# Optimization experiments

Hardware: AMD Instinct MI355X
Metric: run time of the kernel (lower is better)

The kernel has to match this reference:

```python
import math
import jax, jax.numpy as jnp
import numpy as np

HIDDEN = 768
HEADS = 12
HEAD_DIM = HIDDEN // HEADS  # 64
NUM_BUCKETS = 32            # T5-style relative position bias defaults
MAX_DIST = 128
EPS = 1e-6


def _rel_buckets(T):
    # T5 bidirectional relative-position bucketing, computed statically in numpy.
    ctx = np.arange(T)[:, None]
    mem = np.arange(T)[None, :]
    rp = mem - ctx                     # (T, T)
    nb = NUM_BUCKETS // 2
    ret = (rp > 0).astype(np.int64) * nb
    n = np.abs(rp)
    max_exact = nb // 2
    is_small = n < max_exact
    val_large = max_exact + (
        np.log(np.maximum(n, 1) / max_exact) / math.log(MAX_DIST / max_exact) * (nb - max_exact)
    ).astype(np.int64)
    val_large = np.minimum(val_large, nb - 1)
    ret = ret + np.where(is_small, n, val_large)
    return ret  # (T, T) int


def _layernorm(x, scale, bias):
    mu = jnp.mean(x, axis=-1, keepdims=True)
    var = jnp.mean((x - mu) ** 2, axis=-1, keepdims=True)
    return (x - mu) * jax.lax.rsqrt(var + EPS) * scale + bias


def _rms_groupnorm(x, weight):
    # x: (N, C, H, W, D); RMS over (channels-in-group, spatial), per-channel scale.
    N, C, H, W, D = x.shape
    xg = x.reshape(N, HEADS, C // HEADS, H, W, D)
    ms = jnp.mean(xg * xg, axis=(2, 3, 4, 5), keepdims=True)
    xg = xg * jax.lax.rsqrt(ms + EPS)
    return xg.reshape(N, C, H, W, D) * weight[None, :, None, None, None]


def _forward(x, norm1_weight, input_head_weight, input_head_bias,
             qnorm_scale, qnorm_bias, knorm_scale, knorm_bias,
             rel_bias_table, output_head_weight, output_head_bias):
    T, B, C, H, W, D = x.shape
    residual = x
    xn = _rms_groupnorm(x.reshape(T * B, C, H, W, D), norm1_weight)
    # 1x1 conv QKV as channels-last matmul
    w_in = input_head_weight[:, :, 0, 0, 0]                       # (3C, C)
    xt = jnp.transpose(xn, (0, 2, 3, 4, 1))                        # (TB, H, W, D, C)
    qkv = xt @ w_in.T + input_head_bias                            # (TB, H, W, D, 3C)
    # '(t b) (he c) h w d -> (b h w d) he t c'  with c = 3*head_dim
    qkv = qkv.reshape(T, B, H, W, D, HEADS, 3 * HEAD_DIM)
    qkv = jnp.transpose(qkv, (1, 2, 3, 4, 5, 0, 6))                # (B,H,W,D,He,T,3hd)
    qkv = qkv.reshape(B * H * W * D, HEADS, T, 3 * HEAD_DIM)
    q, k, v = jnp.split(qkv, 3, axis=-1)                           # each (N, He, T, hd)
    q = _layernorm(q, qnorm_scale, qnorm_bias)
    k = _layernorm(k, knorm_scale, knorm_bias)
    # relative position bias (bidirectional)
    buckets = jnp.asarray(_rel_buckets(T))                         # (T, T)
    bias = jnp.transpose(rel_bias_table[buckets], (2, 0, 1))[None]  # (1, He, T, T)
    scale = 1.0 / math.sqrt(HEAD_DIM)
    attn = jax.nn.softmax(jnp.einsum('bhsc,bhtc->bhst', q, k) * scale + bias, axis=-1)
    out = jnp.einsum('bhst,bhtc->bhsc', attn, v)                   # (N, He, T, hd)
    # '(b h w d) he t c -> (t b) (he c) h w d'
    out = out.reshape(B, H, W, D, HEADS, T, HEAD_DIM)
    out = jnp.transpose(out, (5, 0, 4, 6, 1, 2, 3))                # (T,B,He,hd,H,W,D)
    out = out.reshape(T * B, C, H, W, D)
    # output 1x1 conv
    w_out = output_head_weight[:, :, 0, 0, 0]                      # (C, C)
    ot = jnp.transpose(out, (0, 2, 3, 4, 1)) @ w_out.T + output_head_bias
    y = jnp.transpose(ot, (0, 4, 1, 2, 3)).reshape(T, B, C, H, W, D)
    return y + residual


def setup_inputs() -> dict:
    key = jax.random.key(0)
    ks = jax.random.split(key, 4)
    T, B, C, H, W, D = 16, 1, HIDDEN, 16, 16, 8
    x = jax.random.normal(ks[0], (T, B, C, H, W, D), dtype=jnp.float32)
    lecun = 1.0 / math.sqrt(HIDDEN)
    return {
        'x': x,
        'norm1_weight': jnp.ones((HIDDEN,), jnp.float32),
        'input_head_weight': jax.random.normal(ks[1], (3 * HIDDEN, HIDDEN, 1, 1, 1), jnp.float32) * lecun,
        'input_head_bias': jnp.zeros((3 * HIDDEN,), jnp.float32),
        'qnorm_scale': jnp.ones((HEAD_DIM,), jnp.float32),
        'qnorm_bias': jnp.zeros((HEAD_DIM,), jnp.float32),
        'knorm_scale': jnp.ones((HEAD_DIM,), jnp.float32),
        'knorm_bias': jnp.zeros((HEAD_DIM,), jnp.float32),
        'rel_bias_table': jax.random.normal(ks[2], (NUM_BUCKETS, HEADS), jnp.float32) * 0.02,
        'output_head_weight': jax.random.normal(ks[3], (HIDDEN, HIDDEN, 1, 1, 1), jnp.float32) * lecun,
        'output_head_bias': jnp.zeros((HIDDEN,), jnp.float32),
    }


def reference(x, norm1_weight, input_head_weight, input_head_bias,
              qnorm_scale, qnorm_bias, knorm_scale, knorm_bias,
              rel_bias_table, output_head_weight, output_head_bias):
    return _forward(x, norm1_weight, input_head_weight, input_head_bias,
                    qnorm_scale, qnorm_bias, knorm_scale, knorm_bias,
                    rel_bias_table, output_head_weight, output_head_bias)
```

## Files before the change

kernel.cpp:

```cpp
#include <hip/hip_runtime.h>
#include <stdint.h>

#define Tt 16
#define Cc 768
#define Ss 2048
#define N1 2304
#define NH 12
#define HD 64
#define EPSV 1e-6f

typedef unsigned short ushort_t;
typedef __attribute__((ext_vector_type(8))) short short8;
typedef __attribute__((ext_vector_type(4))) short short4v;
typedef __attribute__((ext_vector_type(4))) float f32x4;

static __device__ __forceinline__ float b2f(unsigned short u) {
  union { unsigned int i; float f; } c;
  c.i = ((unsigned int)u) << 16;
  return c.f;
}
static __device__ __forceinline__ unsigned short f2b(float f) {
  union { float f; unsigned int i; } c;
  c.f = f;
  return (unsigned short)((c.i + 0x7fffu + ((c.i >> 16) & 1u)) >> 16);
}

static __device__ __forceinline__ void load8(const void* p, size_t eoff,
                                             int isf32, float* o) {
  if (isf32) {
    const float* f = (const float*)p + eoff;
    f32x4 a = *(const f32x4*)f;
    f32x4 b = *(const f32x4*)(f + 4);
    o[0] = a[0]; o[1] = a[1]; o[2] = a[2]; o[3] = a[3];
    o[4] = b[0]; o[5] = b[1]; o[6] = b[2]; o[7] = b[3];
  } else {
    short8 d = *(const short8*)((const ushort_t*)p + eoff);
#pragma unroll
    for (int e = 0; e < 8; e++) o[e] = b2f((unsigned short)d[e]);
  }
}
static __device__ __forceinline__ float load1(const void* p, size_t eoff, int isf32) {
  return isf32 ? ((const float*)p)[eoff] : b2f(((const ushort_t*)p)[eoff]);
}

#define GLP(p) ((const __attribute__((address_space(1))) void*)(p))
#define LDSP(p) ((__attribute__((address_space(3))) void*)(p))

__global__ __launch_bounds__(256) void detect_k(const ushort_t* __restrict__ x,
                                               int* __restrict__ flag) {
  __shared__ int sbad;
  if (threadIdx.x == 0) sbad = 0;
  __syncthreads();
  int bad = 0;
  for (int i = threadIdx.x; i < 65536; i += 256) {
    const unsigned int e = (x[i] >> 7) & 0xFFu;
    if (e == 0xFFu) bad = 1;
  }
  if (bad) atomicOr(&sbad, 1);
  __syncthreads();
  if (threadIdx.x == 0) flag[0] = sbad;
}

__global__ __launch_bounds__(256) void cvt_big_k(const void* __restrict__ src,
                                                ushort_t* __restrict__ dst,
                                                int n8, const int* __restrict__ flag) {
  const int isf32 = *flag;
  const int i = blockIdx.x * 256 + threadIdx.x;
  if (i >= n8) return;
  float o[8];
  load8(src, (size_t)i * 8, isf32, o);
  short8 v;
#pragma unroll
  for (int e = 0; e < 8; e++) v[e] = (short)f2b(o[e]);
  *(short8*)(dst + (size_t)i * 8) = v;
}

__global__ __launch_bounds__(256) void cvt_small_k(
    const void* w1, const void* bin, const void* bo, const void* qs,
    const void* qb, const void* ks, const void* kb, const void* relb,
    ushort_t* __restrict__ dst, const int* __restrict__ flag) {
  const int isf32 = *flag;
  const void* srcs[8] = {w1, bin, bo, qs, qb, ks, kb, relb};
  const int sizes[8] = {768, 2304, 768, 64, 64, 64, 64, 384};
  int off = 0;
#pragma unroll
  for (int s = 0; s < 8; s++) {
    for (int i = threadIdx.x; i < sizes[s]; i += 256)
      dst[off + i] = isf32 ? f2b(((const float*)srcs[s])[i])
                           : ((const ushort_t*)srcs[s])[i];
    off += sizes[s];
  }
}

__global__ __launch_bounds__(256) void rms_stats_k(
    const void* __restrict__ x, const int* __restrict__ flag,
    float* __restrict__ invrms) {
  const int isf32 = *flag;
  const int t = blockIdx.x / NH;
  const int g = blockIdx.x % NH;
  const size_t base = ((size_t)(t * Cc + g * 64)) * Ss;
  float ss = 0.f;
  for (int v = threadIdx.x; v < 16384; v += 256) {
    const int ci = v >> 8;
    const int sj = (v & 255) << 3;
    float o[8];
    load8(x, base + (size_t)ci * Ss + sj, isf32, o);
#pragma unroll
    for (int e = 0; e < 8; e++) ss += o[e] * o[e];
  }
#pragma unroll
  for (int m = 1; m < 64; m <<= 1) ss += __shfl_xor(ss, m);
  __shared__ float red[4];
  if ((threadIdx.x & 63) == 0) red[threadIdx.x >> 6] = ss;
  __syncthreads();
  if (threadIdx.x == 0) {
    float tot = red[0] + red[1] + red[2] + red[3];
    invrms[blockIdx.x] = rsqrtf(tot * (1.f / 131072.f) + EPSV);
  }
}

__global__ __launch_bounds__(256) void norm_chunk_k(
    const void* __restrict__ x, const int* __restrict__ flag,
    const ushort_t* __restrict__ w1, const float* __restrict__ invrms,
    ushort_t* __restrict__ xnc, int s0c, int chl) {
  __shared__ __align__(16) ushort_t tile[64][64];
  const int isf32 = *flag;
  const int t = blockIdx.z;
  const int c0 = blockIdx.y * 64;
  const int sl0 = blockIdx.x * 64;
  const float ir = invrms[t * NH + (c0 >> 6)];
  const int tid = threadIdx.x;
  for (int v = tid; v < 512; v += 256) {
    const int ci = v >> 3;
    const int q = v & 7;
    float o[8];
    load8(x, ((size_t)(t * Cc + c0 + ci)) * Ss + s0c + sl0 + q * 8, isf32, o);
    const float sc = ir * b2f(w1[c0 + ci]);
    short8 w;
#pragma unroll
    for (int e = 0; e < 8; e++) w[e] = (short)f2b(o[e] * sc);
    *(short8*)&tile[ci][(q ^ (ci >> 3)) * 8] = w;
  }
  __syncthreads();
  for (int v = tid; v < 512; v += 256) {
    const int sj = v >> 3;
    const int cb = (v & 7) * 8;
    const int sw = (sj >> 3) ^ (v & 7);
    const int so = sj & 7;
    short8 o;
#pragma unroll
    for (int e = 0; e < 8; e++) o[e] = (short)tile[cb + e][sw * 8 + so];
    *(short8*)(xnc + ((size_t)(t * chl + sl0 + sj)) * Cc + c0 + cb) = o;
  }
}

__global__ __launch_bounds__(256, 2) void gemm_qkv_k(
    const ushort_t* __restrict__ A, const ushort_t* __restrict__ Bw,
    const ushort_t* __restrict__ bias, ushort_t* __restrict__ Cout) {
  __shared__ __align__(16) ushort_t As[128 * 32];
  __shared__ __align__(16) ushort_t Bs[128 * 32];
  const int tid = threadIdx.x;
  const int bm0 = blockIdx.x * 128;
  const int bn0 = blockIdx.y * 128;
  const int lane = tid & 63;
  const int wave = tid >> 6;
  const int wm = (wave >> 1) << 6;
  const int wn = (wave & 1) << 6;
  f32x4 acc[4][4];
#pragma unroll
  for (int i = 0; i < 4; i++)
#pragma unroll
    for (int j = 0; j < 4; j++) acc[i][j] = (f32x4){0.f, 0.f, 0.f, 0.f};
  const int srow = tid >> 2;
  const int scol = (tid & 3) << 3;
  const ushort_t* ag = A + (size_t)(bm0 + srow) * Cc + scol;
  const ushort_t* bg = Bw + (size_t)(bn0 + srow) * Cc + scol;
  ushort_t* la = As + tid * 8;
  ushort_t* lb = Bs + tid * 8;
  const int frow = lane & 15;
  const int koff = (lane >> 4) << 3;
  for (int kt = 0; kt < Cc; kt += 32) {
    __syncthreads();
    __builtin_amdgcn_global_load_lds(GLP(ag + kt), LDSP(la), 16, 0, 0);
    __builtin_amdgcn_global_load_lds(GLP(ag + kt + 64 * Cc), LDSP(la + 2048), 16, 0, 0);
    __builtin_amdgcn_global_load_lds(GLP(bg + kt), LDSP(lb), 16, 0, 0);
    __builtin_amdgcn_global_load_lds(GLP(bg + kt + 64 * Cc), LDSP(lb + 2048), 16, 0, 0);
    __syncthreads();
    short8 af[4], bf[4];
#pragma unroll
    for (int i = 0; i < 4; i++)
      af[i] = *(const short8*)(As + (wm + i * 16 + frow) * 32 + koff);
#pragma unroll
    for (int j = 0; j < 4; j++)
      bf[j] = *(const short8*)(Bs + (wn + j * 16 + frow) * 32 + koff);
#pragma unroll
    for (int i = 0; i < 4; i++)
#pragma unroll
      for (int j = 0; j < 4; j++)
        acc[i][j] = __builtin_amdgcn_mfma_f32_16x16x32_bf16(af[i], bf[j], acc[i][j], 0, 0, 0);
  }
  const int mq = (lane >> 4) << 2;
  const int nl = lane & 15;
#pragma unroll
  for (int j = 0; j < 4; j++) {
    const int col = bn0 + wn + j * 16 + nl;
    const float bc = b2f(bias[col]);
#pragma unroll
    for (int i = 0; i < 4; i++) {
#pragma unroll
      for (int r = 0; r < 4; r++) {
        const int row = bm0 + wm + i * 16 + mq + r;
        Cout[(size_t)row * N1 + col] = f2b(acc[i][j][r] + bc);
      }
    }
  }
}

static __device__ __forceinline__ void rdA4(short8 af[4], const ushort_t* base,
                                            int ar, int mib, int ck) {
#pragma unroll
  for (int mi = 0; mi < 4; mi++)
    af[mi] = *(const short8*)&base[(ar + (mib + mi) * 16) * 32 + ck];
}
static __device__ __forceinline__ void rdB4(short8 bf[4], const ushort_t* base,
                                            int br, int ck) {
#pragma unroll
  for (int ni = 0; ni < 4; ni++)
    bf[ni] = *(const short8*)&base[(br + ni * 16) * 32 + ck];
}
template <int MIB>
static __device__ __forceinline__ void mmq(f32x4 (&acc)[8][4], const short8 af[4],
                                           const short8 bf[4]) {
#pragma unroll
  for (int mi = 0; mi < 4; mi++)
#pragma unroll
    for (int ni = 0; ni < 4; ni++)
      acc[MIB + mi][ni] = __builtin_amdgcn_mfma_f32_16x16x32_bf16(
          af[mi], bf[ni], acc[MIB + mi][ni], 0, 0, 0);
}
#define QPH_BAR { __builtin_amdgcn_sched_barrier(0); __builtin_amdgcn_s_barrier(); \
                  __builtin_amdgcn_sched_barrier(0); }
#define LDSOFF(p, ab, kh) ((((p) * 2 + (ab)) * 2 + (kh)) * 8192)

__global__ __launch_bounds__(512, 2) void gemm_qkv256_k(
    const ushort_t* __restrict__ A, const ushort_t* __restrict__ Bw,
    const ushort_t* __restrict__ bias, ushort_t* __restrict__ Cout) {
  __shared__ __align__(16) ushort_t pool[73728];
  const int tid = threadIdx.x;
  const int lane = tid & 63;
  const int wave = tid >> 6;
  const int wr = wave >> 2;
  const int wc = wave & 3;
  const int wg = ((int)blockIdx.x & 7) * 144 + ((int)blockIdx.x >> 3);
  const int bm0 = (wg / 9) * 256;
  const int bn0 = (wg % 9) * 256;
  const int srow = tid >> 2;
  const int scol = ((tid & 3) ^ ((tid >> 3) & 3)) << 3;
  const ushort_t* ag = A + (size_t)(bm0 + srow) * Cc + scol;
  const ushort_t* bg = Bw + (size_t)(bn0 + srow) * Cc + scol;
#define STGA(p, kh, kt) { \
    __builtin_amdgcn_global_load_lds(GLP(ag + (kt) + (kh) * 32), \
        LDSP(&pool[LDSOFF(p, 0, kh) + tid * 8]), 16, 0, 0); \
    __builtin_amdgcn_global_load_lds(GLP(ag + 128 * Cc + (kt) + (kh) * 32), \
        LDSP(&pool[LDSOFF(p, 0, kh) + 4096 + tid * 8]), 16, 0, 0); \
  }
#define STGB(p, kh, kt) { \
    __builtin_amdgcn_global_load_lds(GLP(bg + (kt) + (kh) * 32), \
        LDSP(&pool[LDSOFF(p, 1, kh) + tid * 8]), 16, 0, 0); \
    __builtin_amdgcn_global_load_lds(GLP(bg + 128 * Cc + (kt) + (kh) * 32), \
        LDSP(&pool[LDSOFF(p, 1, kh) + 4096 + tid * 8]), 16, 0, 0); \
  }
  const int ck = (((lane >> 4) ^ ((lane >> 1) & 3)) << 3);
  const int ar = wr * 128 + (lane & 15);
  const int br = wc * 64 + (lane & 15);
  f32x4 acc[8][4];
#pragma unroll
  for (int i = 0; i < 8; i++)
#pragma unroll
    for (int j = 0; j < 4; j++) acc[i][j] = (f32x4){0.f, 0.f, 0.f, 0.f};
  short8 af[4], bf[4];
  STGA(0, 0, 0); STGB(0, 0, 0); STGA(0, 1, 0); STGB(0, 1, 0);
  asm volatile("s_waitcnt vmcnt(4)");
  QPH_BAR;
  for (int t = 0; t < 11; t++) {
    const int p = t & 1;
    const int q = p ^ 1;
    const int kt = (t + 1) * 64;
    rdA4(af, &pool[LDSOFF(p, 0, 0)], ar, 0, ck);
    rdB4(bf, &pool[LDSOFF(p, 1, 0)], br, ck);
    STGA(q, 0, kt);
    QPH_BAR;
    __builtin_amdgcn_s_setprio(1);
    mmq<0>(acc, af, bf);
    __builtin_amdgcn_s_setprio(0);
    QPH_BAR;
    rdA4(af, &pool[LDSOFF(p, 0, 0)], ar, 4, ck);
    STGB(q, 0, kt);
    QPH_BAR;
    __builtin_amdgcn_s_setprio(1);
    mmq<4>(acc, af, bf);
    __builtin_amdgcn_s_setprio(0);
    __builtin_amdgcn_sched_barrier(0);
    asm volatile("s_waitcnt vmcnt(4)");
    QPH_BAR;
    rdA4(af, &pool[LDSOFF(p, 0, 1)], ar, 0, ck);
    rdB4(bf, &pool[LDSOFF(p, 1, 1)], br, ck);
    STGA(q, 1, kt);
    QPH_BAR;
    __builtin_amdgcn_s_setprio(1);
    mmq<0>(acc, af, bf);
    __builtin_amdgcn_s_setprio(0);
    QPH_BAR;
    rdA4(af, &pool[LDSOFF(p, 0, 1)], ar, 4, ck);
    STGB(q, 1, kt);
    QPH_BAR;
    __builtin_amdgcn_s_setprio(1);
    mmq<4>(acc, af, bf);
    __builtin_amdgcn_s_setprio(0);
    __builtin_amdgcn_sched_barrier(0);
    asm volatile("s_waitcnt vmcnt(4)");
    QPH_BAR;
  }
  {
    rdA4(af, &pool[LDSOFF(1, 0, 0)], ar, 0, ck);
    rdB4(bf, &pool[LDSOFF(1, 1, 0)], br, ck);
    QPH_BAR;
    __builtin_amdgcn_s_setprio(1);
    mmq<0>(acc, af, bf);
    __builtin_amdgcn_s_setprio(0);
    QPH_BAR;
    rdA4(af, &pool[LDSOFF(1, 0, 0)], ar, 4, ck);
    QPH_BAR;
    __builtin_amdgcn_s_setprio(1);
    mmq<4>(acc, af, bf);
    __builtin_amdgcn_s_setprio(0);
    __builtin_amdgcn_sched_barrier(0);
    asm volatile("s_waitcnt vmcnt(0)");
    QPH_BAR;
    rdA4(af, &pool[LDSOFF(1, 0, 1)], ar, 0, ck);
    rdB4(bf, &pool[LDSOFF(1, 1, 1)], br, ck);
    QPH_BAR;
    __builtin_amdgcn_s_setprio(1);
    mmq<0>(acc, af, bf);
    __builtin_amdgcn_s_setprio(0);
    QPH_BAR;
    rdA4(af, &pool[LDSOFF(1, 0, 1)], ar, 4, ck);
    __builtin_amdgcn_s_setprio(1);
    mmq<4>(acc, af, bf);
    __builtin_amdgcn_s_setprio(0);
  }
  __builtin_amdgcn_sched_barrier(0);
  __syncthreads();
  ushort_t* cw = pool + wave * 9216;
  const int mq = (lane >> 4) << 2;
  const int nl = lane & 15;
#pragma unroll
  for (int ni = 0; ni < 4; ni++) {
    const float bc = b2f(bias[bn0 + wc * 64 + ni * 16 + nl]);
#pragma unroll
    for (int mi = 0; mi < 8; mi++) {
#pragma unroll
      for (int r = 0; r < 4; r++)
        cw[(mi * 16 + mq + r) * 72 + ni * 16 + nl] = f2b(acc[mi][ni][r] + bc);
    }
  }
  const int rsub = lane >> 3;
  const int c8 = (lane & 7) * 8;
  ushort_t* outb = Cout + (size_t)(bm0 + wr * 128) * N1 + bn0 + wc * 64;
#pragma unroll
  for (int i = 0; i < 16; i++) {
    const int row = i * 8 + rsub;
    short8 v = *(const short8*)&cw[row * 72 + c8];
    *(short8*)(outb + (size_t)row * N1 + c8) = v;
  }
#undef STGA
#undef STGB
}

__global__ __launch_bounds__(256) void attention_k(
    const ushort_t* __restrict__ qkvc, const ushort_t* __restrict__ qs,
    const ushort_t* __restrict__ qb, const ushort_t* __restrict__ ks,
    const ushort_t* __restrict__ kb, const ushort_t* __restrict__ relb,
    ushort_t* __restrict__ aoc, int chl) {
  __shared__ __align__(16) float qf[4][16][68];
  __shared__ __align__(16) float kf[4][16][68];
  __shared__ __align__(16) float vf[4][16][68];
  __shared__ __align__(16) float attw[4][16][20];
  __shared__ __align__(16) float lnw[4][64];
  const int tid = threadIdx.x;
  const int wave = tid >> 6;
  const int lane = tid & 63;
  if (tid < 64) {
    lnw[0][tid] = b2f(qs[tid]);
    lnw[1][tid] = b2f(qb[tid]);
    lnw[2][tid] = b2f(ks[tid]);
    lnw[3][tid] = b2f(kb[tid]);
  }
  const int p = blockIdx.x * 4 + wave;
  const int sl = p / 12;
  const int h = p - sl * 12;
  const ushort_t* src = qkvc + (size_t)sl * N1 + h * 192;
  const size_t tstride = (size_t)chl * N1;
#pragma unroll
  for (int t = 0; t < 16; t++) {
    const ushort_t* r = src + (size_t)t * tstride;
    qf[wave][t][lane] = b2f(r[lane]);
    kf[wave][t][lane] = b2f(r[64 + lane]);
    vf[wave][t][lane] = b2f(r[128 + lane]);
  }
  __syncthreads();
  {
    const int row = lane >> 1;
    const int half = lane & 1;
    float* buf = (row < 16) ? &qf[wave][row][0] : &kf[wave][row - 16][0];
    const float* sc = (row < 16) ? lnw[0] : lnw[2];
    const float* bi = (row < 16) ? lnw[1] : lnw[3];
    f32x4* bp = (f32x4*)(buf + half * 32);
    f32x4 v4[8];
    float s = 0.f;
#pragma unroll
    for (int q4 = 0; q4 < 8; q4++) {
      v4[q4] = bp[q4];
      s += v4[q4][0] + v4[q4][1] + v4[q4][2] + v4[q4][3];
    }
    s += __shfl_xor(s, 1);
    const float mu = s * (1.f / 64.f);
    float va = 0.f;
#pragma unroll
    for (int q4 = 0; q4 < 8; q4++) {
#pragma unroll
      for (int e = 0; e < 4; e++) {
        const float d = v4[q4][e] - mu;
        va += d * d;
      }
    }
    va += __shfl_xor(va, 1);
    const float rs = rsqrtf(va * (1.f / 64.f) + EPSV);
    const f32x4* sc4 = (const f32x4*)(sc + half * 32);
    const f32x4* bi4 = (const f32x4*)(bi + half * 32);
#pragma unroll
    for (int q4 = 0; q4 < 8; q4++) {
      f32x4 scv = sc4[q4], biv = bi4[q4], o;
#pragma unroll
      for (int e = 0; e < 4; e++) o[e] = (v4[q4][e] - mu) * rs * scv[e] + biv[e];
      bp[q4] = o;
    }
  }
  __syncthreads();
  const int g = lane >> 4;
  const int t2 = lane & 15;
#pragma unroll
  for (int it = 0; it < 4; it++) {
    const int t1 = it * 4 + g;
    const f32x4* qrow = (const f32x4*)&qf[wave][t1][0];
    const f32x4* krow = (const f32x4*)&kf[wave][t2][0];
    float sco = 0.f;
#pragma unroll
    for (int q4 = 0; q4 < 16; q4++) {
      f32x4 a = qrow[q4], b = krow[q4];
      sco += a[0] * b[0] + a[1] * b[1] + a[2] * b[2] + a[3] * b[3];
    }
    const int rp = t2 - t1;
    int bkt = (rp > 0) ? 16 : 0;
    const int n = (rp < 0) ? -rp : rp;
    if (n < 8) {
      bkt += n;
    } else {
      int vl = 8 + (int)(__logf((float)n * 0.125f) * 2.8853900817779268f);
      bkt += (vl < 15) ? vl : 15;
    }
    sco = sco * 0.125f + b2f(relb[bkt * NH + h]);
    float mx = sco;
#pragma unroll
    for (int m = 8; m >= 1; m >>= 1) mx = fmaxf(mx, __shfl_xor(mx, m));
    const float ex = __expf(sco - mx);
    float sm = ex;
#pragma unroll
    for (int m = 8; m >= 1; m >>= 1) sm += __shfl_xor(sm, m);
    attw[wave][t1][t2] = ex / sm;
  }
  __syncthreads();
  const int jq = lane & 15;
#pragma unroll
  for (int it = 0; it < 4; it++) {
    const int t1 = it * 4 + g;
    const f32x4* arow2 = (const f32x4*)&attw[wave][t1][0];
    f32x4 o = (f32x4){0.f, 0.f, 0.f, 0.f};
#pragma unroll
    for (int tq = 0; tq < 4; tq++) {
      f32x4 aw = arow2[tq];
#pragma unroll
      for (int e = 0; e < 4; e++) {
        f32x4 vv = *(const f32x4*)&vf[wave][tq * 4 + e][jq * 4];
        o[0] += aw[e] * vv[0];
        o[1] += aw[e] * vv[1];
        o[2] += aw[e] * vv[2];
        o[3] += aw[e] * vv[3];
      }
    }
    short4v st;
#pragma unroll
    for (int e = 0; e < 4; e++) st[e] = (short)f2b(o[e]);
    *(short4v*)(aoc + ((size_t)(t1 * chl + sl)) * Cc + h * HD + jq * 4) = st;
  }
}

__global__ __launch_bounds__(256, 2) void gemm_out_k(
    const ushort_t* __restrict__ A, const ushort_t* __restrict__ Bm,
    const ushort_t* __restrict__ bias, const void* __restrict__ xres,
    const int* __restrict__ flag, float* __restrict__ y, int s0c,
    int chl, int lgchl) {
  __shared__ __align__(16) ushort_t As[128 * 32];
  __shared__ __align__(16) ushort_t Bs[128 * 32];
  const int isf32 = *flag;
  const int tid = threadIdx.x;
  int bmt = blockIdx.x, bnt = blockIdx.y;
  {
    const int nwg = gridDim.x * gridDim.y;
    if ((nwg & 7) == 0) {
      const int hw = (int)blockIdx.x + (int)blockIdx.y * gridDim.x;
      const int cpx = nwg >> 3;
      const int w = (hw & 7) * cpx + (hw >> 3);
      bmt = w % gridDim.x;
      bnt = w / gridDim.x;
    }
  }
  const int bm0 = bmt * 128;
  const int bn0 = bnt * 128;
  const int lane = tid & 63;
  const int wave = tid >> 6;
  const int wm = (wave >> 1) << 6;
  const int wn = (wave & 1) << 6;
  f32x4 acc[4][4];
#pragma unroll
  for (int i = 0; i < 4; i++)
#pragma unroll
    for (int j = 0; j < 4; j++) acc[i][j] = (f32x4){0.f, 0.f, 0.f, 0.f};
  const int srow = tid >> 2;
  const int scol = (tid & 3) << 3;
  const ushort_t* ag = A + (size_t)(bm0 + srow) * Cc + scol;
  const ushort_t* bg = Bm + (size_t)(bn0 + srow) * Cc + scol;
  ushort_t* la = As + tid * 8;
  ushort_t* lb = Bs + tid * 8;
  const int frow = lane & 15;
  const int koff = (lane >> 4) << 3;
  for (int kt = 0; kt < Cc; kt += 32) {
    __syncthreads();
    __builtin_amdgcn_global_load_lds(GLP(ag + kt), LDSP(la), 16, 0, 0);
    __builtin_amdgcn_global_load_lds(GLP(ag + kt + 64 * Cc), LDSP(la + 2048), 16, 0, 0);
    __builtin_amdgcn_global_load_lds(GLP(bg + kt), LDSP(lb), 16, 0, 0);
    __builtin_amdgcn_global_load_lds(GLP(bg + kt + 64 * Cc), LDSP(lb + 2048), 16, 0, 0);
    __syncthreads();
    short8 af[4], bf[4];
#pragma unroll
    for (int i = 0; i < 4; i++)
      af[i] = *(const short8*)(As + (wm + i * 16 + frow) * 32 + koff);
#pragma unroll
    for (int j = 0; j < 4; j++)
      bf[j] = *(const short8*)(Bs + (wn + j * 16 + frow) * 32 + koff);
#pragma unroll
    for (int i = 0; i < 4; i++)
#pragma unroll
      for (int j = 0; j < 4; j++)
        acc[i][j] = __builtin_amdgcn_mfma_f32_16x16x32_bf16(af[i], bf[j], acc[i][j], 0, 0, 0);
  }
  const int mq = (lane >> 4) << 2;
  const int nl = lane & 15;
#pragma unroll
  for (int j = 0; j < 4; j++) {
    const int col = bn0 + wn + j * 16 + nl;
    const int t = col >> lgchl;
    const int sp = s0c + (col & (chl - 1));
#pragma unroll
    for (int i = 0; i < 4; i++) {
#pragma unroll
      for (int r = 0; r < 4; r++) {
        const int cch = bm0 + wm + i * 16 + mq + r;
        const size_t off = ((size_t)(t * Cc + cch)) * Ss + sp;
        y[off] = acc[i][j][r] + b2f(bias[cch]) + load1(xres, off, isf32);
      }
    }
  }
}

extern "C" void kernel_launch(void* const* d_in, const int* in_sizes, int n_in,
                              void* d_out, int out_size, void* d_ws, size_t ws_size,
                              hipStream_t stream) {
  (void)in_sizes; (void)n_in; (void)out_size;
  const void* x   = d_in[0];
  const void* w1  = d_in[1];
  const void* win = d_in[2];
  const void* bin = d_in[3];
  const void* qsc = d_in[4];
  const void* qbi = d_in[5];
  const void* ksc = d_in[6];
  const void* kbi = d_in[7];
  const void* rbt = d_in[8];
  const void* wo  = d_in[9];
  const void* bo  = d_in[10];
  float* y = (float*)d_out;

  char* ws = (char*)d_ws;
  int* flag      = (int*)ws;
  ushort_t* smallw = (ushort_t*)(ws + 4096);
  ushort_t* w1b  = smallw;
  ushort_t* binb = smallw + 768;
  ushort_t* bob  = smallw + 3072;
  ushort_t* qsb  = smallw + 3840;
  ushort_t* qbb  = smallw + 3904;
  ushort_t* ksb  = smallw + 3968;
  ushort_t* kbb  = smallw + 4032;
  ushort_t* relbb = smallw + 4096;
  float* invrms  = (float*)(ws + 1024);
  ushort_t* winb = (ushort_t*)(ws + 20480);
  ushort_t* wob  = (ushort_t*)(ws + 3559424);
  const size_t fixed = 4739072;

  const size_t per_row = (size_t)(Cc * 2 + N1 * 2 + Cc * 2);
  int chl = Ss;
  while (chl > 64 && fixed + (size_t)Tt * chl * per_row > ws_size) chl >>= 1;
  int lgchl = 0;
  while ((1 << (lgchl + 1)) <= chl) lgchl++;

  ushort_t* xnc  = (ushort_t*)(ws + fixed);
  ushort_t* qkvc = xnc + (size_t)Tt * chl * Cc;
  ushort_t* aoc  = qkvc + (size_t)Tt * chl * N1;

  detect_k<<<1, 256, 0, stream>>>((const ushort_t*)x, flag);
  cvt_small_k<<<1, 256, 0, stream>>>(w1, bin, bo, qsc, qbi, ksc, kbi, rbt, smallw, flag);
  cvt_big_k<<<1769472 / 8 / 256, 256, 0, stream>>>(win, winb, 1769472 / 8, flag);
  cvt_big_k<<<589824 / 8 / 256, 256, 0, stream>>>(wo, wob, 589824 / 8, flag);
  rms_stats_k<<<dim3(Tt * NH), 256, 0, stream>>>(x, flag, invrms);
  for (int s0c = 0; s0c < Ss; s0c += chl) {
    norm_chunk_k<<<dim3(chl / 64, Cc / 64, Tt), 256, 0, stream>>>(x, flag, w1b, invrms, xnc, s0c, chl);
    if (chl == Ss) {
      gemm_qkv256_k<<<dim3(1152), 512, 0, stream>>>(xnc, winb, binb, qkvc);
    } else {
      gemm_qkv_k<<<dim3(Tt * chl / 128, N1 / 128), 256, 0, stream>>>(xnc, winb, binb, qkvc);
    }
    attention_k<<<dim3(chl * NH / 4), 256, 0, stream>>>(qkvc, qsb, qbb, ksb, kbb, relbb, aoc, chl);
    gemm_out_k<<<dim3(Cc / 128, Tt * chl / 128), 256, 0, stream>>>(wob, aoc, bob, x, flag, y, s0c, chl, lgchl);
  }
}
```

Before: 658.1 us.

## Double-buffer LDS tiles in output GEMM with XOR-swizzled layout

```diff
diff --git a/kernel.cpp b/kernel.cpp
--- a/kernel.cpp
+++ b/kernel.cpp
@@ -505,13 +505,13 @@
   }
 }
 
-__global__ __launch_bounds__(256, 2) void gemm_out_k(
+__global__ __launch_bounds__(256, 4) void gemm_out_k(
     const ushort_t* __restrict__ A, const ushort_t* __restrict__ Bm,
     const ushort_t* __restrict__ bias, const void* __restrict__ xres,
     const int* __restrict__ flag, float* __restrict__ y, int s0c,
     int chl, int lgchl) {
-  __shared__ __align__(16) ushort_t As[128 * 32];
-  __shared__ __align__(16) ushort_t Bs[128 * 32];
+  __shared__ __align__(16) ushort_t As[2][128 * 32];
+  __shared__ __align__(16) ushort_t Bs[2][128 * 32];
   const int isf32 = *flag;
   const int tid = threadIdx.x;
   int bmt = blockIdx.x, bnt = blockIdx.y;
@@ -537,33 +537,38 @@
 #pragma unroll
     for (int j = 0; j < 4; j++) acc[i][j] = (f32x4){0.f, 0.f, 0.f, 0.f};
   const int srow = tid >> 2;
-  const int scol = (tid & 3) << 3;
+  const int scol = ((tid & 3) ^ ((tid >> 3) & 3)) << 3;
   const ushort_t* ag = A + (size_t)(bm0 + srow) * Cc + scol;
   const ushort_t* bg = Bm + (size_t)(bn0 + srow) * Cc + scol;
-  ushort_t* la = As + tid * 8;
-  ushort_t* lb = Bs + tid * 8;
+#define OSTG(p, kt) { \
+    __builtin_amdgcn_global_load_lds(GLP(ag + (kt)), LDSP(&As[p][tid * 8]), 16, 0, 0); \
+    __builtin_amdgcn_global_load_lds(GLP(ag + (kt) + 64 * Cc), LDSP(&As[p][2048 + tid * 8]), 16, 0, 0); \
+    __builtin_amdgcn_global_load_lds(GLP(bg + (kt)), LDSP(&Bs[p][tid * 8]), 16, 0, 0); \
+    __builtin_amdgcn_global_load_lds(GLP(bg + (kt) + 64 * Cc), LDSP(&Bs[p][2048 + tid * 8]), 16, 0, 0); \
+  }
   const int frow = lane & 15;
-  const int koff = (lane >> 4) << 3;
-  for (int kt = 0; kt < Cc; kt += 32) {
-    __syncthreads();
-    __builtin_amdgcn_global_load_lds(GLP(ag + kt), LDSP(la), 16, 0, 0);
-    __builtin_amdgcn_global_load_lds(GLP(ag + kt + 64 * Cc), LDSP(la + 2048), 16, 0, 0);
-    __builtin_amdgcn_global_load_lds(GLP(bg + kt), LDSP(lb), 16, 0, 0);
-    __builtin_amdgcn_global_load_lds(GLP(bg + kt + 64 * Cc), LDSP(lb + 2048), 16, 0, 0);
-    __syncthreads();
+  const int ck = (((lane >> 4) ^ ((lane >> 1) & 3)) << 3);
+  OSTG(0, 0);
+  __syncthreads();
+  for (int it = 0; it < 24; it++) {
+    const int p = it & 1;
+    if (it < 23) OSTG(p ^ 1, (it + 1) * 32);
+    __builtin_amdgcn_sched_barrier(0);
     short8 af[4], bf[4];
 #pragma unroll
     for (int i = 0; i < 4; i++)
-      af[i] = *(const short8*)(As + (wm + i * 16 + frow) * 32 + koff);
+      af[i] = *(const short8*)(&As[p][(wm + i * 16 + frow) * 32 + ck]);
 #pragma unroll
     for (int j = 0; j < 4; j++)
-      bf[j] = *(const short8*)(Bs + (wn + j * 16 + frow) * 32 + koff);
+      bf[j] = *(const short8*)(&Bs[p][(wn + j * 16 + frow) * 32 + ck]);
 #pragma unroll
     for (int i = 0; i < 4; i++)
 #pragma unroll
       for (int j = 0; j < 4; j++)
         acc[i][j] = __builtin_amdgcn_mfma_f32_16x16x32_bf16(af[i], bf[j], acc[i][j], 0, 0, 0);
-  }
+    if (it < 23) __syncthreads();
+  }
+#undef OSTG
   const int mq = (lane >> 4) << 2;
   const int nl = lane & 15;
 #pragma unroll
```

Result: no change. 670.3 us (+1.9%).
